# Performance work log

Hardware: AMD Instinct MI355X
Metric: run time of the kernel (lower is better)

## Reference

```python
import jax, jax.numpy as jnp
import numpy as np

B, N, IN_DIM, L = 4, 512, 256, 128


def setup_inputs() -> dict:
    key = jax.random.key(0)
    k1, k2, k3, k4 = jax.random.split(key, 4)
    x = jax.random.normal(k1, (B, N, IN_DIM), dtype=jnp.float32)
    adj = jnp.ones((B, N, N), dtype=jnp.float32)
    box_num = jax.random.randint(k2, (B, 1), 0, N)  # (B,1) int
    # learned params
    W = jax.random.normal(k3, (L, IN_DIM), dtype=jnp.float32) * 0.05  # projection (no bias)
    a = jax.random.uniform(k4, (L,), dtype=jnp.float32)  # adjacency vector, U(0,1)
    return {"x": x, "adj": adj, "box_num": box_num, "W": W, "a": a}


def reference(x, adj, box_num, W, a):
    Bn, Nn, _ = x.shape
    x_hat = jnp.einsum('bnd,ld->bnl', x, W)  # (B,N,L)
    # dynamic mask: -1 where either node is padding, 0 otherwise (B,N,N)
    valid = jnp.arange(Nn)[None, :] < box_num  # (B,N) bool
    pair = valid[:, None, :] & valid[:, :, None]  # (B,N,N)
    mask = jnp.where(pair, 0.0, -1.0).astype(x.dtype)
    # (|x_i - x_j| + mask) . a  ==  |x_i - x_j| . a  +  mask * sum(a)
    diff = jnp.abs(x_hat[:, :, None, :] - x_hat[:, None, :, :])  # (B,N,N,L) big intermediate
    dist = jnp.einsum('bijd,d->bij', diff, a) + mask * jnp.sum(a)
    out = jax.nn.leaky_relu(dist)  # negative_slope 0.01 matches torch default
    out = out - jnp.max(out, axis=-1, keepdims=True)
    soft = adj * jnp.exp(out)
    soft = soft / jnp.sum(soft, axis=-1, keepdims=True) + 1e-10
    return soft
```

## Files before the change

kernel.cpp:

```cpp
#include <hip/hip_runtime.h>
#include <hip/hip_fp16.h>
#include <math.h>

namespace {

constexpr int B_ = 4;
constexpr int N_ = 512;
constexpr int D_ = 256;
constexpr int L_ = 128;
constexpr int L2_ = L_ / 2;
constexpr int TI = 4;

typedef _Float16 v2h __attribute__((ext_vector_type(2)));
typedef float v4f __attribute__((ext_vector_type(4)));

__global__ __launch_bounds__(256) void proj_kernel(
    const float* __restrict__ x, const float* __restrict__ W,
    const float* __restrict__ a, unsigned* __restrict__ xs_u) {
  const int bid = blockIdx.x;
  const int xcd = bid & 7;
  const int b = xcd >> 1;
  const int tile = ((xcd & 1) << 6) + (bid >> 3);
  const int l0 = (tile >> 3) * 8;
  const int n0 = (tile & 7) * 64;

  const int t = threadIdx.x;

  __shared__ float wl_s[8 * 256];
  __shared__ float xl[2][64 * 129];

  const int n = t & 63;
  const int lg = t >> 6;

  {
    const float4* __restrict__ Wsrc =
        reinterpret_cast<const float4*>(W + (size_t)l0 * D_);
    float4* wdst = reinterpret_cast<float4*>(wl_s);
#pragma unroll
    for (int k = 0; k < 2; ++k) wdst[t + k * 256] = Wsrc[t + k * 256];
  }
  {
    const v4f* __restrict__ xsrc =
        reinterpret_cast<const v4f*>(x + ((size_t)(b * N_ + n0)) * D_);
#pragma unroll
    for (int k = 0; k < 16; ++k) {
      const int f = t + k * 256;
      const int sn = f >> 6;
      const int sq = f & 63;
      const v4f v = __builtin_nontemporal_load(&xsrc[f]);
      float* dst = &xl[sq >> 5][sn * 129 + (sq & 31) * 4];
      dst[0] = v.x; dst[1] = v.y; dst[2] = v.z; dst[3] = v.w;
    }
  }
  __syncthreads();

  float acc0 = 0.f, acc1 = 0.f;
  const float4* __restrict__ w4 = reinterpret_cast<const float4*>(wl_s);
#pragma unroll 4
  for (int d4g = 0; d4g < 64; ++d4g) {
    const float* __restrict__ xr = &xl[d4g >> 5][n * 129 + (d4g & 31) * 4];
    const float x0 = xr[0];
    const float x1 = xr[1];
    const float x2 = xr[2];
    const float x3 = xr[3];
    const float4 w0 = w4[(lg * 2 + 0) * 64 + d4g];
    const float4 w1 = w4[(lg * 2 + 1) * 64 + d4g];
    acc0 += x0 * w0.x + x1 * w0.y + x2 * w0.z + x3 * w0.w;
    acc1 += x0 * w1.x + x1 * w1.y + x2 * w1.z + x3 * w1.w;
  }

  const int lbase = l0 + lg * 2;
  const float s0 = acc0 * a[lbase + 0];
  const float s1 = acc1 * a[lbase + 1];
  const auto p01 = __builtin_amdgcn_cvt_pkrtz(s0, s1);
  xs_u[((size_t)b * L2_ + (lbase >> 1)) * N_ + n0 + n] =
      __builtin_bit_cast(unsigned, p01);
}

__global__ __launch_bounds__(512, 4) void dist_softmax_kernel(
    const unsigned* __restrict__ xs_u, const float* __restrict__ adj,
    const int* __restrict__ box_num, const float* __restrict__ a,
    float* __restrict__ out) {
  const int bid = blockIdx.x;
  const int xcd = bid & 7;
  const int b = xcd >> 1;
  const int tile = ((xcd & 1) << 6) + (bid >> 3);
  const int i0 = tile * TI;

  const int t = threadIdx.x;
  const int j = t;
  const int lane = t & 63;
  const int wid = t >> 6;
  const int bn = box_num[b];
  const unsigned* __restrict__ xs_b = xs_u + (size_t)b * L2_ * N_;

  __shared__ float red[8][TI];
  __shared__ float rsinv_s[TI];

  float sum_a;
  {
    float sa = a[lane] + a[lane + 64];
#pragma unroll
    for (int off = 1; off < 64; off <<= 1) sa += __shfl_xor(sa, off);
    sum_a = sa;
  }

  unsigned xiA[TI];
#pragma unroll
  for (int r = 0; r < TI; ++r) {
    xiA[r] = xs_b[lane * N_ + i0 + r];
  }

  unsigned xj[64];
#pragma unroll
  for (int u = 0; u < 64; ++u) {
    xj[u] = xs_b[u * N_ + j];
  }

  float acc[TI];
#pragma unroll
  for (int r = 0; r < TI; ++r) acc[r] = 0.f;

  const v2h one2 = {(_Float16)1.0f, (_Float16)1.0f};

#pragma unroll
  for (int u = 0; u < 64; ++u) {
    const unsigned xjw = xj[u];
#pragma unroll
    for (int r = 0; r < TI; ++r) {
      const unsigned s = __builtin_amdgcn_readlane(xiA[r], u);
      const v2h d = __builtin_bit_cast(v2h, s) -
                    __builtin_bit_cast(v2h, xjw);
      const unsigned du = __builtin_bit_cast(unsigned, d) & 0x7FFF7FFFu;
      acc[r] = __builtin_amdgcn_fdot2(__builtin_bit_cast(v2h, du), one2,
                                      acc[r], false);
    }
  }

  const bool vj = j < bn;
  float e[TI];
  const float* __restrict__ adjp = adj + ((size_t)(b * N_ + i0)) * N_ + j;
#pragma unroll
  for (int r = 0; r < TI; ++r) {
    const bool vi = (i0 + r) < bn;
    const float d = acc[r] - ((vi && vj) ? 0.f : sum_a);
    const float val = d >= 0.f ? d : 0.01f * d;
    const float av = __builtin_nontemporal_load(&adjp[(size_t)r * N_]);
    e[r] = av * __expf(val - 64.0f);
  }

  {
    float wsum[TI];
#pragma unroll
    for (int r = 0; r < TI; ++r) {
      float s = e[r];
#pragma unroll
      for (int off = 1; off < 64; off <<= 1) s += __shfl_xor(s, off);
      wsum[r] = s;
    }
    if (lane == 0) {
#pragma unroll
      for (int r = 0; r < TI; ++r) red[wid][r] = wsum[r];
    }
  }
  __syncthreads();
  if (t < TI) {
    float s = red[0][t];
#pragma unroll
    for (int w = 1; w < 8; ++w) s += red[w][t];
    rsinv_s[t] = 1.0f / s;
  }
  __syncthreads();

  float* __restrict__ op = out + ((size_t)(b * N_ + i0)) * N_ + j;
#pragma unroll
  for (int r = 0; r < TI; ++r) {
    __builtin_nontemporal_store(e[r] * rsinv_s[r] + 1e-10f,
                                &op[(size_t)r * N_]);
  }
}

}

extern "C" void kernel_launch(void* const* d_in, const int* in_sizes, int n_in,
                              void* d_out, int out_size, void* d_ws,
                              size_t ws_size, hipStream_t stream) {
  const float* x = (const float*)d_in[0];
  const float* adj = (const float*)d_in[1];
  const int* box_num = (const int*)d_in[2];
  const float* W = (const float*)d_in[3];
  const float* a = (const float*)d_in[4];
  float* out = (float*)d_out;
  unsigned* xs_u = (unsigned*)d_ws;

  proj_kernel<<<512, 256, 0, stream>>>(x, W, a, xs_u);
  dist_softmax_kernel<<<512, 512, 0, stream>>>(xs_u, adj, box_num, a, out);
}
```

Baseline: 24.96 us.

## Split L reduction across two thread groups with 8 rows per block

The distance kernel now handles 8 query rows per block using 1024 threads, with the two 512-thread halves each covering half of the L dimension. Partial sums are exchanged through shared memory, and each half finishes softmax for 4 rows. The xi values now come from shared memory instead of readlane broadcasts, and each thread loads only 32 xj registers, which lowers register pressure and doubles reuse of each xj load. The cost is an extra barrier, the cross-group exchange, and half as many blocks.

```diff
diff --git a/kernel.cpp b/kernel.cpp
--- a/kernel.cpp
+++ b/kernel.cpp
@@ -9,7 +9,7 @@
 constexpr int D_ = 256;
 constexpr int L_ = 128;
 constexpr int L2_ = L_ / 2;
-constexpr int TI = 4;
+constexpr int TI = 8;
 
 typedef _Float16 v2h __attribute__((ext_vector_type(2)));
 typedef float v4f __attribute__((ext_vector_type(4)));
@@ -77,25 +77,32 @@
       __builtin_bit_cast(unsigned, p01);
 }
 
-__global__ __launch_bounds__(512, 4) void dist_softmax_kernel(
+__global__ __launch_bounds__(1024) void dist_softmax_kernel(
     const unsigned* __restrict__ xs_u, const float* __restrict__ adj,
     const int* __restrict__ box_num, const float* __restrict__ a,
     float* __restrict__ out) {
   const int bid = blockIdx.x;
   const int xcd = bid & 7;
   const int b = xcd >> 1;
-  const int tile = ((xcd & 1) << 6) + (bid >> 3);
+  const int tile = ((xcd & 1) << 5) + (bid >> 3);
   const int i0 = tile * TI;
 
   const int t = threadIdx.x;
-  const int j = t;
+  const int g = t >> 9;
+  const int j = t & 511;
   const int lane = t & 63;
   const int wid = t >> 6;
   const int bn = box_num[b];
   const unsigned* __restrict__ xs_b = xs_u + (size_t)b * L2_ * N_;
 
-  __shared__ float red[8][TI];
-  __shared__ float rsinv_s[TI];
+  __shared__ unsigned xi_s[L2_ * TI];
+  __shared__ float cross[2][512][4];
+  __shared__ float red[16][4];
+  __shared__ float rsinv_s[2][4];
+
+  if (t < L2_ * TI) {
+    xi_s[t] = xs_b[(t >> 3) * N_ + i0 + (t & 7)];
+  }
 
   float sum_a;
   {
@@ -104,32 +111,32 @@
     for (int off = 1; off < 64; off <<= 1) sa += __shfl_xor(sa, off);
     sum_a = sa;
   }
-
-  unsigned xiA[TI];
-#pragma unroll
-  for (int r = 0; r < TI; ++r) {
-    xiA[r] = xs_b[lane * N_ + i0 + r];
-  }
-
-  unsigned xj[64];
-#pragma unroll
-  for (int u = 0; u < 64; ++u) {
-    xj[u] = xs_b[u * N_ + j];
-  }
+  __syncthreads();
 
   float acc[TI];
 #pragma unroll
   for (int r = 0; r < TI; ++r) acc[r] = 0.f;
 
   const v2h one2 = {(_Float16)1.0f, (_Float16)1.0f};
-
-#pragma unroll
-  for (int u = 0; u < 64; ++u) {
+  const uint4* __restrict__ xi4 = reinterpret_cast<const uint4*>(xi_s);
+  const int u0 = g * 32;
+
+  unsigned xj[32];
+#pragma unroll
+  for (int u = 0; u < 32; ++u) {
+    xj[u] = xs_b[(u0 + u) * N_ + j];
+  }
+
+#pragma unroll
+  for (int u = 0; u < 32; ++u) {
     const unsigned xjw = xj[u];
+    const uint4 xiA = xi4[(u0 + u) * 2];
+    const uint4 xiB = xi4[(u0 + u) * 2 + 1];
+    const unsigned xiw[8] = {xiA.x, xiA.y, xiA.z, xiA.w,
+                             xiB.x, xiB.y, xiB.z, xiB.w};
 #pragma unroll
     for (int r = 0; r < TI; ++r) {
-      const unsigned s = __builtin_amdgcn_readlane(xiA[r], u);
-      const v2h d = __builtin_bit_cast(v2h, s) -
+      const v2h d = __builtin_bit_cast(v2h, xiw[r]) -
                     __builtin_bit_cast(v2h, xjw);
       const unsigned du = __builtin_bit_cast(unsigned, d) & 0x7FFF7FFFu;
       acc[r] = __builtin_amdgcn_fdot2(__builtin_bit_cast(v2h, du), one2,
@@ -137,46 +144,63 @@
     }
   }
 
+  {
+    float4 c;
+    c.x = acc[(1 - g) * 4 + 0];
+    c.y = acc[(1 - g) * 4 + 1];
+    c.z = acc[(1 - g) * 4 + 2];
+    c.w = acc[(1 - g) * 4 + 3];
+    *reinterpret_cast<float4*>(&cross[g][j][0]) = c;
+  }
+  __syncthreads();
+
   const bool vj = j < bn;
-  float e[TI];
-  const float* __restrict__ adjp = adj + ((size_t)(b * N_ + i0)) * N_ + j;
-#pragma unroll
-  for (int r = 0; r < TI; ++r) {
-    const bool vi = (i0 + r) < bn;
-    const float d = acc[r] - ((vi && vj) ? 0.f : sum_a);
-    const float val = d >= 0.f ? d : 0.01f * d;
-    const float av = __builtin_nontemporal_load(&adjp[(size_t)r * N_]);
-    e[r] = av * __expf(val - 64.0f);
-  }
-
-  {
-    float wsum[TI];
-#pragma unroll
-    for (int r = 0; r < TI; ++r) {
-      float s = e[r];
+  float e[4];
+  const float* __restrict__ adjp =
+      adj + ((size_t)(b * N_ + i0 + g * 4)) * N_ + j;
+  {
+    const float4 c = *reinterpret_cast<const float4*>(&cross[1 - g][j][0]);
+    const float oth[4] = {c.x, c.y, c.z, c.w};
+#pragma unroll
+    for (int q = 0; q < 4; ++q) {
+      const int row = i0 + g * 4 + q;
+      const float dtot = acc[g * 4 + q] + oth[q] -
+                         (((row < bn) && vj) ? 0.f : sum_a);
+      const float val = dtot >= 0.f ? dtot : 0.01f * dtot;
+      const float av = __builtin_nontemporal_load(&adjp[(size_t)q * N_]);
+      e[q] = av * __expf(val - 64.0f);
+    }
+  }
+
+  {
+    float ws[4];
+#pragma unroll
+    for (int q = 0; q < 4; ++q) {
+      float s = e[q];
 #pragma unroll
       for (int off = 1; off < 64; off <<= 1) s += __shfl_xor(s, off);
-      wsum[r] = s;
+      ws[q] = s;
     }
     if (lane == 0) {
 #pragma unroll
-      for (int r = 0; r < TI; ++r) red[wid][r] = wsum[r];
-    }
-  }
-  __syncthreads();
-  if (t < TI) {
-    float s = red[0][t];
-#pragma unroll
-    for (int w = 1; w < 8; ++w) s += red[w][t];
-    rsinv_s[t] = 1.0f / s;
-  }
-  __syncthreads();
-
-  float* __restrict__ op = out + ((size_t)(b * N_ + i0)) * N_ + j;
-#pragma unroll
-  for (int r = 0; r < TI; ++r) {
-    __builtin_nontemporal_store(e[r] * rsinv_s[r] + 1e-10f,
-                                &op[(size_t)r * N_]);
+      for (int q = 0; q < 4; ++q) red[wid][q] = ws[q];
+    }
+  }
+  __syncthreads();
+  if (t < 8) {
+    const int g2 = t >> 2, q = t & 3;
+    float s = red[g2 * 8][q];
+#pragma unroll
+    for (int w = 1; w < 8; ++w) s += red[g2 * 8 + w][q];
+    rsinv_s[g2][q] = 1.0f / s;
+  }
+  __syncthreads();
+
+  float* __restrict__ op = out + ((size_t)(b * N_ + i0 + g * 4)) * N_ + j;
+#pragma unroll
+  for (int q = 0; q < 4; ++q) {
+    __builtin_nontemporal_store(e[q] * rsinv_s[g][q] + 1e-10f,
+                                &op[(size_t)q * N_]);
   }
 }
 
@@ -194,5 +218,5 @@
   unsigned* xs_u = (unsigned*)d_ws;
 
   proj_kernel<<<512, 256, 0, stream>>>(x, W, a, xs_u);
-  dist_softmax_kernel<<<512, 512, 0, stream>>>(xs_u, adj, box_num, a, out);
-}
+  dist_softmax_kernel<<<256, 1024, 0, stream>>>(xs_u, adj, box_num, a, out);
+}
```

Measured after the change: 24.56 us. No clear change (-1.6%).
